# Performance work log

Hardware: AMD Instinct MI355X
Metric: run time of the kernel (lower is better)

Reference implementation:

```python
import jax, jax.numpy as jnp
import numpy as np

T, H, I, E, K, G, TG = 8192, 2048, 1024, 64, 8, 8, 4
ROUTED_SCALE = 2.5


def setup_inputs() -> dict:
    key = jax.random.key(0)
    ks = jax.random.split(key, 7)
    s = 0.02  # weight init scale
    return {
        "hidden_states": jax.random.normal(ks[0], (T, H), jnp.float32),
        "gate_w": jax.random.normal(ks[1], (E, H), jnp.float32) * s,
        "e_bias": jax.random.normal(ks[2], (E,), jnp.float32) * s,
        "w_gate_up": jax.random.normal(ks[3], (E, H, 2 * I), jnp.float32) * s,
        "w_down": jax.random.normal(ks[4], (E, I, H), jnp.float32) * s,
        "shared_gate_up": jax.random.normal(ks[5], (H, 2 * I), jnp.float32) * s,
        "shared_down": jax.random.normal(ks[6], (I, H), jnp.float32) * s,
    }


def silu_and_mul(x):
    g, u = jnp.split(x, 2, axis=-1)
    return jax.nn.silu(g) * u


def grouped_topk(router_logits, e_bias):
    # sigmoid scoring with e_score_correction_bias (DeepSeek-V3 / GLM4-MoE style)
    scores = jax.nn.sigmoid(router_logits)            # [T, E]
    scores_for_choice = scores + e_bias[None, :]
    # group score = sum of top-2 biased scores in each group
    grp = scores_for_choice.reshape(-1, G, E // G)
    group_scores = jax.lax.top_k(grp, 2)[0].sum(-1)   # [T, G]
    _, gidx = jax.lax.top_k(group_scores, TG)         # [T, TG]
    tok = jnp.arange(scores.shape[0])[:, None]
    group_mask = jnp.zeros_like(group_scores, dtype=bool).at[tok, gidx].set(True)
    expert_mask = jnp.repeat(group_mask, E // G, axis=-1)  # [T, E]
    masked = jnp.where(expert_mask, scores_for_choice, -jnp.inf)
    _, topk_ids = jax.lax.top_k(masked, K)            # [T, K]
    # combine weights come from the *unbiased* sigmoid scores
    topk_w = jnp.take_along_axis(scores, topk_ids, axis=-1)
    topk_w = topk_w / jnp.sum(topk_w, axis=-1, keepdims=True)  # renormalize
    return topk_w, topk_ids


def reference(hidden_states, gate_w, e_bias, w_gate_up, w_down,
              shared_gate_up, shared_down):
    x = hidden_states                                  # [T, H]
    # gate runs in fp32
    router_logits = x.astype(jnp.float32) @ gate_w.T   # [T, E]
    topk_w, topk_ids = grouped_topk(router_logits, e_bias)

    # shared expert MLP
    shared_out = silu_and_mul(x @ shared_gate_up) @ shared_down  # [T, H]

    # dense [T, E] combine matrix (top-k sparse in values)
    tok = jnp.arange(x.shape[0])[:, None]
    route = jnp.zeros((x.shape[0], E), x.dtype).at[tok, topk_ids].set(
        topk_w.astype(x.dtype))

    # grouped expert GEMMs via scan over experts (bounds peak memory)
    def body(acc, params):
        w1, w2, rw = params                            # [H,2I], [I,H], [T]
        y = silu_and_mul(x @ w1) @ w2                  # [T, H]
        return acc + rw[:, None] * y, None

    acc0 = jnp.zeros_like(x)
    routed_out, _ = jax.lax.scan(body, acc0, (w_gate_up, w_down, route.T))

    return routed_out * ROUTED_SCALE + shared_out
```

## Files before the change

### kernel.cpp

```cpp
#include <hip/hip_runtime.h>
#include <stdint.h>

#define T_TOK 8192
#define HDIM  2048
#define IDIM  1024
#define NEXP  64
#define KTOP  8
#define TGRP  4
#define TKTOT (T_TOK*KTOP)
#define MAXITEMS 4096
#define RSCALE 2.5f

typedef __attribute__((ext_vector_type(8))) short short8;
typedef __attribute__((ext_vector_type(4))) float f32x4;

#define VMCNT(n) asm volatile("s_waitcnt vmcnt(" #n ")" ::: "memory")
#define BARRIER() asm volatile("s_barrier" ::: "memory")

__device__ __forceinline__ float bf2f(uint16_t u) {
    union { unsigned i; float f; } v; v.i = ((unsigned)u) << 16; return v.f;
}
__device__ __forceinline__ uint16_t f2bf(float f) {
    union { float f; unsigned i; } v; v.f = f;
    unsigned r = (v.i + 0x7FFFu + ((v.i >> 16) & 1u)) >> 16;
    return (uint16_t)r;
}
__device__ __forceinline__ void gload_lds16(const void* g, void* l) {
    __builtin_amdgcn_global_load_lds(
        (const __attribute__((address_space(1))) void*)g,
        (__attribute__((address_space(3))) void*)l, 16, 0, 0);
}
__device__ __forceinline__ int imin(int a, int b) { return a < b ? a : b; }

__global__ __launch_bounds__(256) void k_router(
    const float* __restrict__ x, const float* __restrict__ gw,
    const float* __restrict__ ebias,
    int* __restrict__ topk_ids, float* __restrict__ topk_w,
    int* __restrict__ counts)
{
    __shared__ float xs[16][132];
    __shared__ float wsb[64][133];
    __shared__ float sc[16][65];
    __shared__ float su[16][65];
    const int tid = threadIdx.x;
    const int e = tid & 63;
    const int tg = tid >> 6;
    const long tblk = (long)blockIdx.x * 16;

    float acc0 = 0.f, acc1 = 0.f, acc2 = 0.f, acc3 = 0.f;
    for (int ch = 0; ch < 16; ++ch) {
        const int h0 = ch << 7;
        for (int i = tid; i < 512; i += 256) {
            int r = i >> 5, c4 = (i & 31) << 2;
            float4 v = *(const float4*)(x + (tblk + r) * HDIM + h0 + c4);
            *(float4*)&xs[r][c4] = v;
        }
        for (int i = tid; i < 8192; i += 256) {
            int r = i >> 7, c = i & 127;
            wsb[r][c] = gw[(long)r * HDIM + h0 + c];
        }
        __syncthreads();
        #pragma unroll 8
        for (int hh = 0; hh < 128; ++hh) {
            float wv = wsb[e][hh];
            acc0 += xs[tg][hh] * wv;
            acc1 += xs[tg + 4][hh] * wv;
            acc2 += xs[tg + 8][hh] * wv;
            acc3 += xs[tg + 12][hh] * wv;
        }
        __syncthreads();
    }
    const float be = ebias[e];
    {
        float s;
        s = 1.f / (1.f + expf(-acc0)); su[tg][e] = s;      sc[tg][e] = s + be;
        s = 1.f / (1.f + expf(-acc1)); su[tg + 4][e] = s;  sc[tg + 4][e] = s + be;
        s = 1.f / (1.f + expf(-acc2)); su[tg + 8][e] = s;  sc[tg + 8][e] = s + be;
        s = 1.f / (1.f + expf(-acc3)); su[tg + 12][e] = s; sc[tg + 12][e] = s + be;
    }
    __syncthreads();
    if (tid < 16) {
        const int t = tid;
        float gs[8];
        #pragma unroll
        for (int g = 0; g < 8; ++g) {
            float m1 = -1e30f, m2 = -1e30f;
            #pragma unroll
            for (int j = 0; j < 8; ++j) {
                float v = sc[t][g * 8 + j];
                if (v > m1) { m2 = m1; m1 = v; } else if (v > m2) { m2 = v; }
            }
            gs[g] = m1 + m2;
        }
        int selmask = 0;
        #pragma unroll
        for (int it = 0; it < TGRP; ++it) {
            float best = -1e30f; int bg = 0;
            #pragma unroll
            for (int g = 0; g < 8; ++g)
                if (!((selmask >> g) & 1) && gs[g] > best) { best = gs[g]; bg = g; }
            selmask |= (1 << bg);
        }
        unsigned long long chosen = 0ull;
        int ids[KTOP]; float wv[KTOP]; float wsum = 0.f;
        #pragma unroll
        for (int it = 0; it < KTOP; ++it) {
            float best = -1e30f; int bi = 0;
            for (int ee = 0; ee < 64; ++ee) {
                if (((selmask >> (ee >> 3)) & 1) && !((chosen >> ee) & 1ull)) {
                    float v = sc[t][ee];
                    if (v > best) { best = v; bi = ee; }
                }
            }
            chosen |= (1ull << bi);
            ids[it] = bi; wv[it] = su[t][bi]; wsum += wv[it];
        }
        const float inv = 1.f / wsum;
        #pragma unroll
        for (int k = 0; k < KTOP; ++k) {
            topk_ids[(tblk + t) * KTOP + k] = ids[k];
            topk_w[(tblk + t) * KTOP + k] = wv[k] * inv;
            atomicAdd(&counts[ids[k]], 1);
        }
    }
}

__global__ __launch_bounds__(64) void k_scan2(
    const int* __restrict__ counts, int* offsets, int* cursor,
    int* __restrict__ it_r0, int* __restrict__ it_end,
    int* __restrict__ it_e, int* __restrict__ it_n0, int* __restrict__ nitems)
{
    const int e = threadIdx.x;
    const int c = counts[e];
    int pre = c;
    #pragma unroll
    for (int d = 1; d < 64; d <<= 1) {
        int v = __shfl_up(pre, d, 64);
        if (e >= d) pre += v;
    }
    const int offE = pre - c;
    offsets[e] = offE; cursor[e] = offE;
    const int ntl = (c + 255) >> 8;
    int ipre = ntl;
    #pragma unroll
    for (int d = 1; d < 64; d <<= 1) {
        int v = __shfl_up(ipre, d, 64);
        if (e >= d) ipre += v;
    }
    const int ibase = (ipre - ntl) * 8;
    for (int p = 0; p < 8; ++p)
        for (int t = 0; t < ntl; ++t) {
            int idx = ibase + p * ntl + t;
            it_r0[idx] = offE + t * 256;
            it_end[idx] = offE + c;
            it_e[idx] = e;
            it_n0[idx] = p << 8;
        }
    if (e == 63) *nitems = ibase + ntl * 8;
}

__global__ __launch_bounds__(256) void k_scatter(
    const int* __restrict__ topk_ids, int* cursor,
    int* __restrict__ perm_token, int* __restrict__ slot_of)
{
    int i = blockIdx.x * 256 + threadIdx.x;
    if (i >= TKTOT) return;
    int e = topk_ids[i];
    int pos = atomicAdd(&cursor[e], 1);
    perm_token[pos] = i >> 3;
    slot_of[i] = pos;
}

__global__ __launch_bounds__(256) void k_cvt_bf16(
    const float* __restrict__ in, uint16_t* __restrict__ outp, long n4)
{
    long i = (long)blockIdx.x * 256 + threadIdx.x;
    if (i >= n4) return;
    float4 v = *(const float4*)(in + i * 4);
    uint64_t pk = (uint64_t)f2bf(v.x) | ((uint64_t)f2bf(v.y) << 16)
                | ((uint64_t)f2bf(v.z) << 32) | ((uint64_t)f2bf(v.w) << 48);
    *(uint64_t*)(outp + i * 4) = pk;
}

template<bool INTER>
__global__ __launch_bounds__(256) void k_transpose2(
    const float* __restrict__ src, uint16_t* __restrict__ dst,
    int R, int C, long sStride, long dStride)
{
    __shared__ float tile[64][65];
    const int c0 = blockIdx.x << 6, r0 = blockIdx.y << 6, s = blockIdx.z;
    const float* S = src + (long)s * sStride;
    uint16_t* D = dst + (long)s * dStride;
    const int lc = (threadIdx.x & 15) << 2;
    const int lr = threadIdx.x >> 4;
    #pragma unroll
    for (int p = 0; p < 4; ++p) {
        int y = lr + p * 16;
        float4 v = *(const float4*)(S + (long)(r0 + y) * C + c0 + lc);
        tile[y][lc] = v.x; tile[y][lc + 1] = v.y;
        tile[y][lc + 2] = v.z; tile[y][lc + 3] = v.w;
    }
    __syncthreads();
    const int wc = threadIdx.x >> 3;
    const int wx = (threadIdx.x & 7) << 3;
    #pragma unroll
    for (int p = 0; p < 2; ++p) {
        int c = wc + p * 32;
        short8 v;
        #pragma unroll
        for (int j = 0; j < 8; ++j) v[j] = (short)f2bf(tile[wx + j][c]);
        int cg = c0 + c;
        int rd = INTER ? (((cg & (IDIM - 1)) << 1) + (cg >> 10)) : cg;
        *(short8*)(D + (long)rd * R + r0 + wx) = v;
    }
}

template<bool GATEUP, bool ROUTED>
__global__ __launch_bounds__(512, 2) void k_gemm6(
    const uint16_t* __restrict__ A, const uint16_t* __restrict__ Bw,
    void* __restrict__ OutP,
    const int* __restrict__ perm_token,
    const int* __restrict__ it_r0, const int* __restrict__ it_end,
    const int* __restrict__ it_e, const int* __restrict__ it_n0,
    const int* __restrict__ nitems, int* __restrict__ qcur,
    int Kd, long expStride)
{
    __shared__ char ldsb[4 * 32768];
    __shared__ int s_item;
    const int tid = threadIdx.x, lane = tid & 63, wid = tid >> 6;
    const int wm = wid >> 2, wn = wid & 3;

    const int rchunk = lane >> 2;
    const int swzS = ((lane & 3) ^ ((lane >> 3) & 3)) << 3;
    const int swzR = ((lane >> 4) ^ ((lane >> 1) & 3)) << 4;
    const int aoff = (wm * 128 + (lane & 15)) * 64 + swzR;
    const int boff = (wn * 64 + (lane & 15)) * 64 + swzR;
    const int dstA0 = (wid * 2) * 1024;
    const int dstA1 = (wid * 2 + 1) * 1024;

    const int nKt = Kd >> 5;
    const int NI = ROUTED ? nitems[0] : 0;

    for (;;) {
        int row0, end, n0; long eoff;
        if (ROUTED) {
            __syncthreads();
            if (tid == 0) s_item = atomicAdd(qcur, 1);
            __syncthreads();
            const int it = s_item;
            if (it >= NI) break;
            row0 = it_r0[it]; end = it_end[it]; n0 = it_n0[it];
            eoff = (long)it_e[it] * expStride;
        } else {
            row0 = (int)(blockIdx.x >> 3) << 8;
            end = row0 + 256;
            n0 = (int)(blockIdx.x & 7) << 8;
            eoff = 0;
        }

        const uint16_t *pa0, *pa1, *pb0, *pb1;
        {
            int r0l = wid * 32 + rchunk;
            int r1l = wid * 32 + 16 + rchunk;
            int ra0 = row0 + r0l, ra1 = row0 + r1l;
            if (ROUTED) { ra0 = imin(ra0, end - 1); ra1 = imin(ra1, end - 1); }
            long ga0 = (GATEUP && ROUTED) ? (long)perm_token[ra0] : (long)ra0;
            long ga1 = (GATEUP && ROUTED) ? (long)perm_token[ra1] : (long)ra1;
            pa0 = A + ga0 * Kd + swzS;
            pa1 = A + ga1 * Kd + swzS;
            pb0 = Bw + eoff + (long)(n0 + r0l) * Kd + swzS;
            pb1 = Bw + eoff + (long)(n0 + r1l) * Kd + swzS;
        }

        f32x4 acc[8][4];
        #pragma unroll
        for (int f = 0; f < 8; ++f)
            #pragma unroll
            for (int g = 0; g < 4; ++g) { f32x4 z = {0.f,0.f,0.f,0.f}; acc[f][g] = z; }

        #pragma unroll
        for (int j = 0; j < 3; ++j) {
            char* bb = ldsb + j * 32768;
            gload_lds16(pa0 + (j << 5), bb + dstA0);
            gload_lds16(pa1 + (j << 5), bb + dstA1);
            gload_lds16(pb0 + (j << 5), bb + 16384 + dstA0);
            gload_lds16(pb1 + (j << 5), bb + 16384 + dstA1);
        }

        for (int kt = 0; kt < nKt; ++kt) {
            const char* bb = ldsb + (kt & 3) * 32768;
            char* bs = ldsb + ((kt + 3) & 3) * 32768;
            const bool st = (kt + 3) < nKt;

            VMCNT(8);
            BARRIER();

            short8 fa0 = *(const short8*)(bb + aoff);
            short8 fa1 = *(const short8*)(bb + aoff + 1024);
            short8 fa2 = *(const short8*)(bb + aoff + 2048);
            short8 fa3 = *(const short8*)(bb + aoff + 3072);
            short8 fb0 = *(const short8*)(bb + 16384 + boff);
            short8 fb1 = *(const short8*)(bb + 16384 + boff + 1024);
            short8 fb2 = *(const short8*)(bb + 16384 + boff + 2048);
            short8 fb3 = *(const short8*)(bb + 16384 + boff + 3072);
            if (st) {
                gload_lds16(pa0 + ((kt + 3) << 5), bs + dstA0);
                gload_lds16(pa1 + ((kt + 3) << 5), bs + dstA1);
            }
            BARRIER();
            __builtin_amdgcn_s_setprio(1);
            acc[0][0] = __builtin_amdgcn_mfma_f32_16x16x32_bf16(fa0, fb0, acc[0][0], 0, 0, 0);
            acc[0][1] = __builtin_amdgcn_mfma_f32_16x16x32_bf16(fa0, fb1, acc[0][1], 0, 0, 0);
            acc[0][2] = __builtin_amdgcn_mfma_f32_16x16x32_bf16(fa0, fb2, acc[0][2], 0, 0, 0);
            acc[0][3] = __builtin_amdgcn_mfma_f32_16x16x32_bf16(fa0, fb3, acc[0][3], 0, 0, 0);
            acc[1][0] = __builtin_amdgcn_mfma_f32_16x16x32_bf16(fa1, fb0, acc[1][0], 0, 0, 0);
            acc[1][1] = __builtin_amdgcn_mfma_f32_16x16x32_bf16(fa1, fb1, acc[1][1], 0, 0, 0);
            acc[1][2] = __builtin_amdgcn_mfma_f32_16x16x32_bf16(fa1, fb2, acc[1][2], 0, 0, 0);
            acc[1][3] = __builtin_amdgcn_mfma_f32_16x16x32_bf16(fa1, fb3, acc[1][3], 0, 0, 0);
            acc[2][0] = __builtin_amdgcn_mfma_f32_16x16x32_bf16(fa2, fb0, acc[2][0], 0, 0, 0);
            acc[2][1] = __builtin_amdgcn_mfma_f32_16x16x32_bf16(fa2, fb1, acc[2][1], 0, 0, 0);
            acc[2][2] = __builtin_amdgcn_mfma_f32_16x16x32_bf16(fa2, fb2, acc[2][2], 0, 0, 0);
            acc[2][3] = __builtin_amdgcn_mfma_f32_16x16x32_bf16(fa2, fb3, acc[2][3], 0, 0, 0);
            acc[3][0] = __builtin_amdgcn_mfma_f32_16x16x32_bf16(fa3, fb0, acc[3][0], 0, 0, 0);
            acc[3][1] = __builtin_amdgcn_mfma_f32_16x16x32_bf16(fa3, fb1, acc[3][1], 0, 0, 0);
            acc[3][2] = __builtin_amdgcn_mfma_f32_16x16x32_bf16(fa3, fb2, acc[3][2], 0, 0, 0);
            acc[3][3] = __builtin_amdgcn_mfma_f32_16x16x32_bf16(fa3, fb3, acc[3][3], 0, 0, 0);
            __builtin_amdgcn_s_setprio(0);

            short8 fa4 = *(const short8*)(bb + aoff + 4096);
            short8 fa5 = *(const short8*)(bb + aoff + 5120);
            short8 fa6 = *(const short8*)(bb + aoff + 6144);
            short8 fa7 = *(const short8*)(bb + aoff + 7168);
            if (st) {
                gload_lds16(pb0 + ((kt + 3) << 5), bs + 16384 + dstA0);
                gload_lds16(pb1 + ((kt + 3) << 5), bs + 16384 + dstA1);
            }
            BARRIER();
            __builtin_amdgcn_s_setprio(1);
            acc[4][0] = __builtin_amdgcn_mfma_f32_16x16x32_bf16(fa4, fb0, acc[4][0], 0, 0, 0);
            acc[4][1] = __builtin_amdgcn_mfma_f32_16x16x32_bf16(fa4, fb1, acc[4][1], 0, 0, 0);
            acc[4][2] = __builtin_amdgcn_mfma_f32_16x16x32_bf16(fa4, fb2, acc[4][2], 0, 0, 0);
            acc[4][3] = __builtin_amdgcn_mfma_f32_16x16x32_bf16(fa4, fb3, acc[4][3], 0, 0, 0);
            acc[5][0] = __builtin_amdgcn_mfma_f32_16x16x32_bf16(fa5, fb0, acc[5][0], 0, 0, 0);
            acc[5][1] = __builtin_amdgcn_mfma_f32_16x16x32_bf16(fa5, fb1, acc[5][1], 0, 0, 0);
            acc[5][2] = __builtin_amdgcn_mfma_f32_16x16x32_bf16(fa5, fb2, acc[5][2], 0, 0, 0);
            acc[5][3] = __builtin_amdgcn_mfma_f32_16x16x32_bf16(fa5, fb3, acc[5][3], 0, 0, 0);
            acc[6][0] = __builtin_amdgcn_mfma_f32_16x16x32_bf16(fa6, fb0, acc[6][0], 0, 0, 0);
            acc[6][1] = __builtin_amdgcn_mfma_f32_16x16x32_bf16(fa6, fb1, acc[6][1], 0, 0, 0);
            acc[6][2] = __builtin_amdgcn_mfma_f32_16x16x32_bf16(fa6, fb2, acc[6][2], 0, 0, 0);
            acc[6][3] = __builtin_amdgcn_mfma_f32_16x16x32_bf16(fa6, fb3, acc[6][3], 0, 0, 0);
            acc[7][0] = __builtin_amdgcn_mfma_f32_16x16x32_bf16(fa7, fb0, acc[7][0], 0, 0, 0);
            acc[7][1] = __builtin_amdgcn_mfma_f32_16x16x32_bf16(fa7, fb1, acc[7][1], 0, 0, 0);
            acc[7][2] = __builtin_amdgcn_mfma_f32_16x16x32_bf16(fa7, fb2, acc[7][2], 0, 0, 0);
            acc[7][3] = __builtin_amdgcn_mfma_f32_16x16x32_bf16(fa7, fb3, acc[7][3], 0, 0, 0);
            __builtin_amdgcn_s_setprio(0);
        }

        const int colb = n0 + wn * 64 + (lane & 15);
        const int rowbase = row0 + wm * 128 + ((lane >> 4) << 2);
        if (GATEUP) {
            uint16_t* Oact = (uint16_t*)OutP;
            const bool evenl = ((lane & 1) == 0);
            #pragma unroll
            for (int f = 0; f < 8; ++f)
                #pragma unroll
                for (int g = 0; g < 4; ++g) {
                    f32x4 v = acc[f][g];
                    #pragma unroll
                    for (int r = 0; r < 4; ++r) {
                        float gg = v[r];
                        float uu = __shfl_xor(gg, 1, 64);
                        int row = rowbase + f * 16 + r;
                        if (evenl && (!ROUTED || row < end)) {
                            int jcol = (colb + g * 16) >> 1;
                            float sg = gg / (1.f + __expf(-gg));
                            Oact[(long)row * IDIM + jcol] = f2bf(sg * uu);
                        }
                    }
                }
        } else if (ROUTED) {
            uint16_t* Y = (uint16_t*)OutP;
            #pragma unroll
            for (int f = 0; f < 8; ++f)
                #pragma unroll
                for (int g = 0; g < 4; ++g) {
                    f32x4 v = acc[f][g];
                    #pragma unroll
                    for (int r = 0; r < 4; ++r) {
                        int row = rowbase + f * 16 + r;
                        if (row < end)
                            Y[(long)row * HDIM + colb + g * 16] = f2bf(v[r]);
                    }
                }
        } else {
            float* O = (float*)OutP;
            #pragma unroll
            for (int f = 0; f < 8; ++f)
                #pragma unroll
                for (int g = 0; g < 4; ++g) {
                    f32x4 v = acc[f][g];
                    #pragma unroll
                    for (int r = 0; r < 4; ++r) {
                        int row = rowbase + f * 16 + r;
                        O[(long)row * HDIM + colb + g * 16] = v[r];
                    }
                }
        }
        if (!ROUTED) break;
    }
}

__global__ __launch_bounds__(256) void k_combine(
    float* __restrict__ out, const uint16_t* __restrict__ ybuf,
    const int* __restrict__ slot_of, const float* __restrict__ topk_w)
{
    __shared__ int sl[KTOP];
    __shared__ float sw[KTOP];
    const int t = blockIdx.x, tid = threadIdx.x;
    if (tid < KTOP) {
        sl[tid] = slot_of[t * KTOP + tid];
        sw[tid] = topk_w[t * KTOP + tid] * RSCALE;
    }
    __syncthreads();
    const int h0 = tid << 3;
    float* orow = out + (long)t * HDIM + h0;
    float4 v0 = *(const float4*)(orow);
    float4 v1 = *(const float4*)(orow + 4);
    float a[8] = { v0.x, v0.y, v0.z, v0.w, v1.x, v1.y, v1.z, v1.w };
    #pragma unroll
    for (int k = 0; k < KTOP; ++k) {
        const uint16_t* yr = ybuf + (long)sl[k] * HDIM + h0;
        short8 y = *(const short8*)yr;
        float w = sw[k];
        #pragma unroll
        for (int j = 0; j < 8; ++j)
            a[j] += w * bf2f((uint16_t)y[j]);
    }
    v0.x = a[0]; v0.y = a[1]; v0.z = a[2]; v0.w = a[3];
    v1.x = a[4]; v1.y = a[5]; v1.z = a[6]; v1.w = a[7];
    *(float4*)(orow) = v0;
    *(float4*)(orow + 4) = v1;
}

extern "C" void kernel_launch(void* const* d_in, const int* in_sizes, int n_in,
                              void* d_out, int out_size, void* d_ws, size_t ws_size,
                              hipStream_t stream)
{
    const float* x  = (const float*)d_in[0];
    const float* gw = (const float*)d_in[1];
    const float* eb = (const float*)d_in[2];
    const float* w1 = (const float*)d_in[3];
    const float* w2 = (const float*)d_in[4];
    const float* s1 = (const float*)d_in[5];
    const float* s2 = (const float*)d_in[6];
    float* out = (float*)d_out;
    char* ws = (char*)d_ws;

    size_t off = 0;
    auto take = [&](size_t b) { size_t r = off; off += (b + 255) & ~(size_t)255; return r; };
    const size_t oXBF = take((size_t)T_TOK * HDIM * 2);
    const size_t oACT = take((size_t)TKTOT * IDIM * 2);
    const size_t oASH = take((size_t)T_TOK * IDIM * 2);
    const size_t oW1T = take((size_t)NEXP * 2048 * 2048 * 2);
    const size_t oW2T = take((size_t)NEXP * 2048 * 1024 * 2);
    const size_t oS1T = take((size_t)2048 * 2048 * 2);
    const size_t oS2T = take((size_t)2048 * 1024 * 2);
    const size_t oTKI = take((size_t)TKTOT * 4);
    const size_t oTKW = take((size_t)TKTOT * 4);
    const size_t oSLT = take((size_t)TKTOT * 4);
    const size_t oPRM = take((size_t)TKTOT * 4);
    const size_t oCTL = take(1024);
    const size_t oOFS = take(256);
    const size_t oCUR = take(256);
    const size_t oNT  = take(256);
    const size_t oIR  = take(MAXITEMS * 4);
    const size_t oIE  = take(MAXITEMS * 4);
    const size_t oIX  = take(MAXITEMS * 4);
    const size_t oIN  = take(MAXITEMS * 4);
    (void)ws_size; (void)in_sizes; (void)n_in; (void)out_size;

    uint16_t* xbf  = (uint16_t*)(ws + oXBF);
    uint16_t* act  = (uint16_t*)(ws + oACT);
    uint16_t* ash  = (uint16_t*)(ws + oASH);
    uint16_t* w1t  = (uint16_t*)(ws + oW1T);
    uint16_t* ybuf = (uint16_t*)(ws + oW1T);
    uint16_t* w2t  = (uint16_t*)(ws + oW2T);
    uint16_t* s1t  = (uint16_t*)(ws + oS1T);
    uint16_t* s2t  = (uint16_t*)(ws + oS2T);
    int*   tki  = (int*)(ws + oTKI);
    float* tkw  = (float*)(ws + oTKW);
    int*   slot = (int*)(ws + oSLT);
    int*   prm  = (int*)(ws + oPRM);
    int*   ctl  = (int*)(ws + oCTL);
    int*   ofs  = (int*)(ws + oOFS);
    int*   cur  = (int*)(ws + oCUR);
    int*   nt   = (int*)(ws + oNT);
    int*   ir0  = (int*)(ws + oIR);
    int*   iend = (int*)(ws + oIE);
    int*   ie   = (int*)(ws + oIX);
    int*   in0  = (int*)(ws + oIN);

    hipMemsetAsync(ws + oCTL, 0, 1024, stream);

    k_router<<<T_TOK / 16, 256, 0, stream>>>(x, gw, eb, tki, tkw, ctl);
    k_scan2<<<1, 64, 0, stream>>>(ctl, ofs, cur, ir0, iend, ie, in0, nt);
    k_scatter<<<TKTOT / 256, 256, 0, stream>>>(tki, cur, prm, slot);

    k_cvt_bf16<<<(T_TOK * HDIM / 4 + 255) / 256, 256, 0, stream>>>(x, xbf, (long)T_TOK * HDIM / 4);
    k_transpose2<true ><<<dim3(32, 32, NEXP), 256, 0, stream>>>(w1, w1t, 2048, 2048,
        (long)2048 * 2048, (long)2048 * 2048);
    k_transpose2<false><<<dim3(32, 16, NEXP), 256, 0, stream>>>(w2, w2t, 1024, 2048,
        (long)1024 * 2048, (long)2048 * 1024);
    k_transpose2<true ><<<dim3(32, 32, 1), 256, 0, stream>>>(s1, s1t, 2048, 2048, 0, 0);
    k_transpose2<false><<<dim3(32, 16, 1), 256, 0, stream>>>(s2, s2t, 1024, 2048, 0, 0);

    k_gemm6<true, false><<<dim3(256), 512, 0, stream>>>(
        xbf, s1t, ash, nullptr, nullptr, nullptr, nullptr, nullptr, nullptr, nullptr, 2048, 0);
    k_gemm6<true, true><<<dim3(256), 512, 0, stream>>>(
        xbf, w1t, act, prm, ir0, iend, ie, in0, nt, ctl + 64, 2048, (long)2048 * 2048);
    k_gemm6<false, false><<<dim3(256), 512, 0, stream>>>(
        ash, s2t, out, nullptr, nullptr, nullptr, nullptr, nullptr, nullptr, nullptr, 1024, 0);
    k_gemm6<false, true><<<dim3(256), 512, 0, stream>>>(
        act, w2t, ybuf, nullptr, ir0, iend, ie, in0, nt, ctl + 65, 1024, (long)2048 * 1024);

    k_combine<<<T_TOK, 256, 0, stream>>>(out, ybuf, slot, tkw);
}
```

Baseline: 2.140 ms.

## Shrink GEMM tiles to 128x128 with 256-thread blocks and finer routed work items

Moves the grouped and shared GEMMs from 256x256 tiles on 512-thread blocks to 128x128 tiles on 256-thread blocks. LDS staging and the accumulator arrays are halved, and the routed scheduler splits each expert into 128-row by 128-column items. The aim is less padding waste on experts whose token counts are not multiples of 256, better load balance across CUs, and higher occupancy. The cost is lower arithmetic intensity per tile, with more global and LDS traffic for each MFMA, plus a tail-aware vmcnt wait in the k-loop.

```diff
diff --git a/kernel.cpp b/kernel.cpp
--- a/kernel.cpp
+++ b/kernel.cpp
@@ -8,7 +8,7 @@
 #define KTOP  8
 #define TGRP  4
 #define TKTOT (T_TOK*KTOP)
-#define MAXITEMS 4096
+#define MAXITEMS 12288
 #define RSCALE 2.5f
 
 typedef __attribute__((ext_vector_type(8))) short short8;
@@ -125,7 +125,7 @@
     }
 }
 
-__global__ __launch_bounds__(64) void k_scan2(
+__global__ __launch_bounds__(64) void k_scan3(
     const int* __restrict__ counts, int* offsets, int* cursor,
     int* __restrict__ it_r0, int* __restrict__ it_end,
     int* __restrict__ it_e, int* __restrict__ it_n0, int* __restrict__ nitems)
@@ -140,23 +140,23 @@
     }
     const int offE = pre - c;
     offsets[e] = offE; cursor[e] = offE;
-    const int ntl = (c + 255) >> 8;
+    const int ntl = (c + 127) >> 7;
     int ipre = ntl;
     #pragma unroll
     for (int d = 1; d < 64; d <<= 1) {
         int v = __shfl_up(ipre, d, 64);
         if (e >= d) ipre += v;
     }
-    const int ibase = (ipre - ntl) * 8;
-    for (int p = 0; p < 8; ++p)
+    const int ibase = (ipre - ntl) * 16;
+    for (int p = 0; p < 16; ++p)
         for (int t = 0; t < ntl; ++t) {
             int idx = ibase + p * ntl + t;
-            it_r0[idx] = offE + t * 256;
+            it_r0[idx] = offE + t * 128;
             it_end[idx] = offE + c;
             it_e[idx] = e;
-            it_n0[idx] = p << 8;
-        }
-    if (e == 63) *nitems = ibase + ntl * 8;
+            it_n0[idx] = p << 7;
+        }
+    if (e == 63) *nitems = ibase + ntl * 16;
 }
 
 __global__ __launch_bounds__(256) void k_scatter(
@@ -216,7 +216,7 @@
 }
 
 template<bool GATEUP, bool ROUTED>
-__global__ __launch_bounds__(512, 2) void k_gemm6(
+__global__ __launch_bounds__(256, 2) void k_gemm7(
     const uint16_t* __restrict__ A, const uint16_t* __restrict__ Bw,
     void* __restrict__ OutP,
     const int* __restrict__ perm_token,
@@ -225,18 +225,18 @@
     const int* __restrict__ nitems, int* __restrict__ qcur,
     int Kd, long expStride)
 {
-    __shared__ char ldsb[4 * 32768];
+    __shared__ char ldsb[4 * 16384];
     __shared__ int s_item;
     const int tid = threadIdx.x, lane = tid & 63, wid = tid >> 6;
-    const int wm = wid >> 2, wn = wid & 3;
+    const int wm = wid >> 1, wn = wid & 1;
 
     const int rchunk = lane >> 2;
     const int swzS = ((lane & 3) ^ ((lane >> 3) & 3)) << 3;
     const int swzR = ((lane >> 4) ^ ((lane >> 1) & 3)) << 4;
-    const int aoff = (wm * 128 + (lane & 15)) * 64 + swzR;
+    const int aoff = (wm * 64 + (lane & 15)) * 64 + swzR;
     const int boff = (wn * 64 + (lane & 15)) * 64 + swzR;
-    const int dstA0 = (wid * 2) * 1024;
-    const int dstA1 = (wid * 2 + 1) * 1024;
+    const int dst0 = (wid * 2) * 1024;
+    const int dst1 = (wid * 2 + 1) * 1024;
 
     const int nKt = Kd >> 5;
     const int NI = ROUTED ? nitems[0] : 0;
@@ -252,16 +252,16 @@
             row0 = it_r0[it]; end = it_end[it]; n0 = it_n0[it];
             eoff = (long)it_e[it] * expStride;
         } else {
-            row0 = (int)(blockIdx.x >> 3) << 8;
-            end = row0 + 256;
-            n0 = (int)(blockIdx.x & 7) << 8;
+            row0 = (int)(blockIdx.x >> 4) << 7;
+            end = row0 + 128;
+            n0 = (int)(blockIdx.x & 15) << 7;
             eoff = 0;
         }
 
         const uint16_t *pa0, *pa1, *pb0, *pb1;
         {
             int r0l = wid * 32 + rchunk;
-            int r1l = wid * 32 + 16 + rchunk;
+            int r1l = r0l + 16;
             int ra0 = row0 + r0l, ra1 = row0 + r1l;
             if (ROUTED) { ra0 = imin(ra0, end - 1); ra1 = imin(ra1, end - 1); }
             long ga0 = (GATEUP && ROUTED) ? (long)perm_token[ra0] : (long)ra0;
@@ -272,40 +272,41 @@
             pb1 = Bw + eoff + (long)(n0 + r1l) * Kd + swzS;
         }
 
-        f32x4 acc[8][4];
-        #pragma unroll
-        for (int f = 0; f < 8; ++f)
+        f32x4 acc[4][4];
+        #pragma unroll
+        for (int f = 0; f < 4; ++f)
             #pragma unroll
             for (int g = 0; g < 4; ++g) { f32x4 z = {0.f,0.f,0.f,0.f}; acc[f][g] = z; }
 
         #pragma unroll
         for (int j = 0; j < 3; ++j) {
-            char* bb = ldsb + j * 32768;
-            gload_lds16(pa0 + (j << 5), bb + dstA0);
-            gload_lds16(pa1 + (j << 5), bb + dstA1);
-            gload_lds16(pb0 + (j << 5), bb + 16384 + dstA0);
-            gload_lds16(pb1 + (j << 5), bb + 16384 + dstA1);
+            char* bb = ldsb + j * 16384;
+            gload_lds16(pa0 + (j << 5), bb + dst0);
+            gload_lds16(pa1 + (j << 5), bb + dst1);
+            gload_lds16(pb0 + (j << 5), bb + 8192 + dst0);
+            gload_lds16(pb1 + (j << 5), bb + 8192 + dst1);
         }
 
         for (int kt = 0; kt < nKt; ++kt) {
-            const char* bb = ldsb + (kt & 3) * 32768;
-            char* bs = ldsb + ((kt + 3) & 3) * 32768;
-            const bool st = (kt + 3) < nKt;
-
-            VMCNT(8);
+            if (kt + 2 < nKt)      VMCNT(8);
+            else if (kt + 1 < nKt) VMCNT(4);
+            else                   VMCNT(0);
             BARRIER();
-
+            const char* bb = ldsb + (kt & 3) * 16384;
+            char* bs = ldsb + ((kt + 3) & 3) * 16384;
             short8 fa0 = *(const short8*)(bb + aoff);
             short8 fa1 = *(const short8*)(bb + aoff + 1024);
             short8 fa2 = *(const short8*)(bb + aoff + 2048);
             short8 fa3 = *(const short8*)(bb + aoff + 3072);
-            short8 fb0 = *(const short8*)(bb + 16384 + boff);
-            short8 fb1 = *(const short8*)(bb + 16384 + boff + 1024);
-            short8 fb2 = *(const short8*)(bb + 16384 + boff + 2048);
-            short8 fb3 = *(const short8*)(bb + 16384 + boff + 3072);
-            if (st) {
-                gload_lds16(pa0 + ((kt + 3) << 5), bs + dstA0);
-                gload_lds16(pa1 + ((kt + 3) << 5), bs + dstA1);
+            short8 fb0 = *(const short8*)(bb + 8192 + boff);
+            short8 fb1 = *(const short8*)(bb + 8192 + boff + 1024);
+            short8 fb2 = *(const short8*)(bb + 8192 + boff + 2048);
+            short8 fb3 = *(const short8*)(bb + 8192 + boff + 3072);
+            if (kt + 3 < nKt) {
+                gload_lds16(pa0 + ((kt + 3) << 5), bs + dst0);
+                gload_lds16(pa1 + ((kt + 3) << 5), bs + dst1);
+                gload_lds16(pb0 + ((kt + 3) << 5), bs + 8192 + dst0);
+                gload_lds16(pb1 + ((kt + 3) << 5), bs + 8192 + dst1);
             }
             BARRIER();
             __builtin_amdgcn_s_setprio(1);
@@ -326,43 +327,15 @@
             acc[3][2] = __builtin_amdgcn_mfma_f32_16x16x32_bf16(fa3, fb2, acc[3][2], 0, 0, 0);
             acc[3][3] = __builtin_amdgcn_mfma_f32_16x16x32_bf16(fa3, fb3, acc[3][3], 0, 0, 0);
             __builtin_amdgcn_s_setprio(0);
-
-            short8 fa4 = *(const short8*)(bb + aoff + 4096);
-            short8 fa5 = *(const short8*)(bb + aoff + 5120);
-            short8 fa6 = *(const short8*)(bb + aoff + 6144);
-            short8 fa7 = *(const short8*)(bb + aoff + 7168);
-            if (st) {
-                gload_lds16(pb0 + ((kt + 3) << 5), bs + 16384 + dstA0);
-                gload_lds16(pb1 + ((kt + 3) << 5), bs + 16384 + dstA1);
-            }
-            BARRIER();
-            __builtin_amdgcn_s_setprio(1);
-            acc[4][0] = __builtin_amdgcn_mfma_f32_16x16x32_bf16(fa4, fb0, acc[4][0], 0, 0, 0);
-            acc[4][1] = __builtin_amdgcn_mfma_f32_16x16x32_bf16(fa4, fb1, acc[4][1], 0, 0, 0);
-            acc[4][2] = __builtin_amdgcn_mfma_f32_16x16x32_bf16(fa4, fb2, acc[4][2], 0, 0, 0);
-            acc[4][3] = __builtin_amdgcn_mfma_f32_16x16x32_bf16(fa4, fb3, acc[4][3], 0, 0, 0);
-            acc[5][0] = __builtin_amdgcn_mfma_f32_16x16x32_bf16(fa5, fb0, acc[5][0], 0, 0, 0);
-            acc[5][1] = __builtin_amdgcn_mfma_f32_16x16x32_bf16(fa5, fb1, acc[5][1], 0, 0, 0);
-            acc[5][2] = __builtin_amdgcn_mfma_f32_16x16x32_bf16(fa5, fb2, acc[5][2], 0, 0, 0);
-            acc[5][3] = __builtin_amdgcn_mfma_f32_16x16x32_bf16(fa5, fb3, acc[5][3], 0, 0, 0);
-            acc[6][0] = __builtin_amdgcn_mfma_f32_16x16x32_bf16(fa6, fb0, acc[6][0], 0, 0, 0);
-            acc[6][1] = __builtin_amdgcn_mfma_f32_16x16x32_bf16(fa6, fb1, acc[6][1], 0, 0, 0);
-            acc[6][2] = __builtin_amdgcn_mfma_f32_16x16x32_bf16(fa6, fb2, acc[6][2], 0, 0, 0);
-            acc[6][3] = __builtin_amdgcn_mfma_f32_16x16x32_bf16(fa6, fb3, acc[6][3], 0, 0, 0);
-            acc[7][0] = __builtin_amdgcn_mfma_f32_16x16x32_bf16(fa7, fb0, acc[7][0], 0, 0, 0);
-            acc[7][1] = __builtin_amdgcn_mfma_f32_16x16x32_bf16(fa7, fb1, acc[7][1], 0, 0, 0);
-            acc[7][2] = __builtin_amdgcn_mfma_f32_16x16x32_bf16(fa7, fb2, acc[7][2], 0, 0, 0);
-            acc[7][3] = __builtin_amdgcn_mfma_f32_16x16x32_bf16(fa7, fb3, acc[7][3], 0, 0, 0);
-            __builtin_amdgcn_s_setprio(0);
         }
 
         const int colb = n0 + wn * 64 + (lane & 15);
-        const int rowbase = row0 + wm * 128 + ((lane >> 4) << 2);
+        const int rowbase = row0 + wm * 64 + ((lane >> 4) << 2);
         if (GATEUP) {
             uint16_t* Oact = (uint16_t*)OutP;
             const bool evenl = ((lane & 1) == 0);
             #pragma unroll
-            for (int f = 0; f < 8; ++f)
+            for (int f = 0; f < 4; ++f)
                 #pragma unroll
                 for (int g = 0; g < 4; ++g) {
                     f32x4 v = acc[f][g];
@@ -381,7 +354,7 @@
         } else if (ROUTED) {
             uint16_t* Y = (uint16_t*)OutP;
             #pragma unroll
-            for (int f = 0; f < 8; ++f)
+            for (int f = 0; f < 4; ++f)
                 #pragma unroll
                 for (int g = 0; g < 4; ++g) {
                     f32x4 v = acc[f][g];
@@ -395,7 +368,7 @@
         } else {
             float* O = (float*)OutP;
             #pragma unroll
-            for (int f = 0; f < 8; ++f)
+            for (int f = 0; f < 4; ++f)
                 #pragma unroll
                 for (int g = 0; g < 4; ++g) {
                     f32x4 v = acc[f][g];
@@ -503,7 +476,7 @@
     hipMemsetAsync(ws + oCTL, 0, 1024, stream);
 
     k_router<<<T_TOK / 16, 256, 0, stream>>>(x, gw, eb, tki, tkw, ctl);
-    k_scan2<<<1, 64, 0, stream>>>(ctl, ofs, cur, ir0, iend, ie, in0, nt);
+    k_scan3<<<1, 64, 0, stream>>>(ctl, ofs, cur, ir0, iend, ie, in0, nt);
     k_scatter<<<TKTOT / 256, 256, 0, stream>>>(tki, cur, prm, slot);
 
     k_cvt_bf16<<<(T_TOK * HDIM / 4 + 255) / 256, 256, 0, stream>>>(x, xbf, (long)T_TOK * HDIM / 4);
@@ -514,13 +487,13 @@
     k_transpose2<true ><<<dim3(32, 32, 1), 256, 0, stream>>>(s1, s1t, 2048, 2048, 0, 0);
     k_transpose2<false><<<dim3(32, 16, 1), 256, 0, stream>>>(s2, s2t, 1024, 2048, 0, 0);
 
-    k_gemm6<true, false><<<dim3(256), 512, 0, stream>>>(
+    k_gemm7<true, false><<<dim3(1024), 256, 0, stream>>>(
         xbf, s1t, ash, nullptr, nullptr, nullptr, nullptr, nullptr, nullptr, nullptr, 2048, 0);
-    k_gemm6<true, true><<<dim3(256), 512, 0, stream>>>(
+    k_gemm7<true, true><<<dim3(512), 256, 0, stream>>>(
         xbf, w1t, act, prm, ir0, iend, ie, in0, nt, ctl + 64, 2048, (long)2048 * 2048);
-    k_gemm6<false, false><<<dim3(256), 512, 0, stream>>>(
+    k_gemm7<false, false><<<dim3(1024), 256, 0, stream>>>(
         ash, s2t, out, nullptr, nullptr, nullptr, nullptr, nullptr, nullptr, nullptr, 1024, 0);
-    k_gemm6<false, true><<<dim3(256), 512, 0, stream>>>(
+    k_gemm7<false, true><<<dim3(512), 256, 0, stream>>>(
         act, w2t, ybuf, nullptr, ir0, iend, ie, in0, nt, ctl + 65, 1024, (long)2048 * 1024);
 
     k_combine<<<T_TOK, 256, 0, stream>>>(out, ybuf, slot, tkw);
```

Result: slower. 2.316 ms (+8.2%).

## Use one barrier per k-step and stagger MFMA half-order across waves

Applied to the files above, without the earlier changes.

The GEMM main loop drops from three barriers per k-step to one: all four global-to-LDS prefetches are issued right after the barrier, and the vmcnt wait is tapered in the last iterations so it stays correct when fewer prefetches are in flight. Odd and even waves process the two A-fragment halves in opposite order, which staggers LDS reads against MFMA work across waves. This is meant to cut barrier stalls and LDS read contention. The cost is a larger code body and longer register lifetimes, which could spill at the 2-blocks-per-CU launch bound.

```diff
diff --git a/kernel.cpp b/kernel.cpp
--- a/kernel.cpp
+++ b/kernel.cpp
@@ -216,7 +216,7 @@
 }
 
 template<bool GATEUP, bool ROUTED>
-__global__ __launch_bounds__(512, 2) void k_gemm6(
+__global__ __launch_bounds__(512, 2) void k_gemm8(
     const uint16_t* __restrict__ A, const uint16_t* __restrict__ Bw,
     void* __restrict__ OutP,
     const int* __restrict__ perm_token,
@@ -237,6 +237,7 @@
     const int boff = (wn * 64 + (lane & 15)) * 64 + swzR;
     const int dstA0 = (wid * 2) * 1024;
     const int dstA1 = (wid * 2 + 1) * 1024;
+    const bool oddw = (wid & 1);
 
     const int nKt = Kd >> 5;
     const int NI = ROUTED ? nitems[0] : 0;
@@ -290,70 +291,114 @@
         for (int kt = 0; kt < nKt; ++kt) {
             const char* bb = ldsb + (kt & 3) * 32768;
             char* bs = ldsb + ((kt + 3) & 3) * 32768;
-            const bool st = (kt + 3) < nKt;
-
-            VMCNT(8);
+
+            if (kt + 2 < nKt)      VMCNT(8);
+            else if (kt + 1 < nKt) VMCNT(4);
+            else                   VMCNT(0);
             BARRIER();
-
-            short8 fa0 = *(const short8*)(bb + aoff);
-            short8 fa1 = *(const short8*)(bb + aoff + 1024);
-            short8 fa2 = *(const short8*)(bb + aoff + 2048);
-            short8 fa3 = *(const short8*)(bb + aoff + 3072);
+            if (kt + 3 < nKt) {
+                gload_lds16(pa0 + ((kt + 3) << 5), bs + dstA0);
+                gload_lds16(pa1 + ((kt + 3) << 5), bs + dstA1);
+                gload_lds16(pb0 + ((kt + 3) << 5), bs + 16384 + dstA0);
+                gload_lds16(pb1 + ((kt + 3) << 5), bs + 16384 + dstA1);
+            }
+
             short8 fb0 = *(const short8*)(bb + 16384 + boff);
             short8 fb1 = *(const short8*)(bb + 16384 + boff + 1024);
             short8 fb2 = *(const short8*)(bb + 16384 + boff + 2048);
             short8 fb3 = *(const short8*)(bb + 16384 + boff + 3072);
-            if (st) {
-                gload_lds16(pa0 + ((kt + 3) << 5), bs + dstA0);
-                gload_lds16(pa1 + ((kt + 3) << 5), bs + dstA1);
+
+            if (!oddw) {
+                short8 fa0 = *(const short8*)(bb + aoff);
+                short8 fa1 = *(const short8*)(bb + aoff + 1024);
+                short8 fa2 = *(const short8*)(bb + aoff + 2048);
+                short8 fa3 = *(const short8*)(bb + aoff + 3072);
+                __builtin_amdgcn_s_setprio(1);
+                acc[0][0] = __builtin_amdgcn_mfma_f32_16x16x32_bf16(fa0, fb0, acc[0][0], 0, 0, 0);
+                acc[0][1] = __builtin_amdgcn_mfma_f32_16x16x32_bf16(fa0, fb1, acc[0][1], 0, 0, 0);
+                acc[0][2] = __builtin_amdgcn_mfma_f32_16x16x32_bf16(fa0, fb2, acc[0][2], 0, 0, 0);
+                acc[0][3] = __builtin_amdgcn_mfma_f32_16x16x32_bf16(fa0, fb3, acc[0][3], 0, 0, 0);
+                acc[1][0] = __builtin_amdgcn_mfma_f32_16x16x32_bf16(fa1, fb0, acc[1][0], 0, 0, 0);
+                acc[1][1] = __builtin_amdgcn_mfma_f32_16x16x32_bf16(fa1, fb1, acc[1][1], 0, 0, 0);
+                acc[1][2] = __builtin_amdgcn_mfma_f32_16x16x32_bf16(fa1, fb2, acc[1][2], 0, 0, 0);
+                acc[1][3] = __builtin_amdgcn_mfma_f32_16x16x32_bf16(fa1, fb3, acc[1][3], 0, 0, 0);
+                acc[2][0] = __builtin_amdgcn_mfma_f32_16x16x32_bf16(fa2, fb0, acc[2][0], 0, 0, 0);
+                acc[2][1] = __builtin_amdgcn_mfma_f32_16x16x32_bf16(fa2, fb1, acc[2][1], 0, 0, 0);
+                acc[2][2] = __builtin_amdgcn_mfma_f32_16x16x32_bf16(fa2, fb2, acc[2][2], 0, 0, 0);
+                acc[2][3] = __builtin_amdgcn_mfma_f32_16x16x32_bf16(fa2, fb3, acc[2][3], 0, 0, 0);
+                acc[3][0] = __builtin_amdgcn_mfma_f32_16x16x32_bf16(fa3, fb0, acc[3][0], 0, 0, 0);
+                acc[3][1] = __builtin_amdgcn_mfma_f32_16x16x32_bf16(fa3, fb1, acc[3][1], 0, 0, 0);
+                acc[3][2] = __builtin_amdgcn_mfma_f32_16x16x32_bf16(fa3, fb2, acc[3][2], 0, 0, 0);
+                acc[3][3] = __builtin_amdgcn_mfma_f32_16x16x32_bf16(fa3, fb3, acc[3][3], 0, 0, 0);
+                __builtin_amdgcn_s_setprio(0);
+                short8 fa4 = *(const short8*)(bb + aoff + 4096);
+                short8 fa5 = *(const short8*)(bb + aoff + 5120);
+                short8 fa6 = *(const short8*)(bb + aoff + 6144);
+                short8 fa7 = *(const short8*)(bb + aoff + 7168);
+                __builtin_amdgcn_s_setprio(1);
+                acc[4][0] = __builtin_amdgcn_mfma_f32_16x16x32_bf16(fa4, fb0, acc[4][0], 0, 0, 0);
+                acc[4][1] = __builtin_amdgcn_mfma_f32_16x16x32_bf16(fa4, fb1, acc[4][1], 0, 0, 0);
+                acc[4][2] = __builtin_amdgcn_mfma_f32_16x16x32_bf16(fa4, fb2, acc[4][2], 0, 0, 0);
+                acc[4][3] = __builtin_amdgcn_mfma_f32_16x16x32_bf16(fa4, fb3, acc[4][3], 0, 0, 0);
+                acc[5][0] = __builtin_amdgcn_mfma_f32_16x16x32_bf16(fa5, fb0, acc[5][0], 0, 0, 0);
+                acc[5][1] = __builtin_amdgcn_mfma_f32_16x16x32_bf16(fa5, fb1, acc[5][1], 0, 0, 0);
+                acc[5][2] = __builtin_amdgcn_mfma_f32_16x16x32_bf16(fa5, fb2, acc[5][2], 0, 0, 0);
+                acc[5][3] = __builtin_amdgcn_mfma_f32_16x16x32_bf16(fa5, fb3, acc[5][3], 0, 0, 0);
+                acc[6][0] = __builtin_amdgcn_mfma_f32_16x16x32_bf16(fa6, fb0, acc[6][0], 0, 0, 0);
+                acc[6][1] = __builtin_amdgcn_mfma_f32_16x16x32_bf16(fa6, fb1, acc[6][1], 0, 0, 0);
+                acc[6][2] = __builtin_amdgcn_mfma_f32_16x16x32_bf16(fa6, fb2, acc[6][2], 0, 0, 0);
+                acc[6][3] = __builtin_amdgcn_mfma_f32_16x16x32_bf16(fa6, fb3, acc[6][3], 0, 0, 0);
+                acc[7][0] = __builtin_amdgcn_mfma_f32_16x16x32_bf16(fa7, fb0, acc[7][0], 0, 0, 0);
+                acc[7][1] = __builtin_amdgcn_mfma_f32_16x16x32_bf16(fa7, fb1, acc[7][1], 0, 0, 0);
+                acc[7][2] = __builtin_amdgcn_mfma_f32_16x16x32_bf16(fa7, fb2, acc[7][2], 0, 0, 0);
+                acc[7][3] = __builtin_amdgcn_mfma_f32_16x16x32_bf16(fa7, fb3, acc[7][3], 0, 0, 0);
+                __builtin_amdgcn_s_setprio(0);
+            } else {
+                short8 fa4 = *(const short8*)(bb + aoff + 4096);
+                short8 fa5 = *(const short8*)(bb + aoff + 5120);
+                short8 fa6 = *(const short8*)(bb + aoff + 6144);
+                short8 fa7 = *(const short8*)(bb + aoff + 7168);
+                __builtin_amdgcn_s_setprio(1);
+                acc[4][0] = __builtin_amdgcn_mfma_f32_16x16x32_bf16(fa4, fb0, acc[4][0], 0, 0, 0);
+                acc[4][1] = __builtin_amdgcn_mfma_f32_16x16x32_bf16(fa4, fb1, acc[4][1], 0, 0, 0);
+                acc[4][2] = __builtin_amdgcn_mfma_f32_16x16x32_bf16(fa4, fb2, acc[4][2], 0, 0, 0);
+                acc[4][3] = __builtin_amdgcn_mfma_f32_16x16x32_bf16(fa4, fb3, acc[4][3], 0, 0, 0);
+                acc[5][0] = __builtin_amdgcn_mfma_f32_16x16x32_bf16(fa5, fb0, acc[5][0], 0, 0, 0);
+                acc[5][1] = __builtin_amdgcn_mfma_f32_16x16x32_bf16(fa5, fb1, acc[5][1], 0, 0, 0);
+                acc[5][2] = __builtin_amdgcn_mfma_f32_16x16x32_bf16(fa5, fb2, acc[5][2], 0, 0, 0);
+                acc[5][3] = __builtin_amdgcn_mfma_f32_16x16x32_bf16(fa5, fb3, acc[5][3], 0, 0, 0);
+                acc[6][0] = __builtin_amdgcn_mfma_f32_16x16x32_bf16(fa6, fb0, acc[6][0], 0, 0, 0);
+                acc[6][1] = __builtin_amdgcn_mfma_f32_16x16x32_bf16(fa6, fb1, acc[6][1], 0, 0, 0);
+                acc[6][2] = __builtin_amdgcn_mfma_f32_16x16x32_bf16(fa6, fb2, acc[6][2], 0, 0, 0);
+                acc[6][3] = __builtin_amdgcn_mfma_f32_16x16x32_bf16(fa6, fb3, acc[6][3], 0, 0, 0);
+                acc[7][0] = __builtin_amdgcn_mfma_f32_16x16x32_bf16(fa7, fb0, acc[7][0], 0, 0, 0);
+                acc[7][1] = __builtin_amdgcn_mfma_f32_16x16x32_bf16(fa7, fb1, acc[7][1], 0, 0, 0);
+                acc[7][2] = __builtin_amdgcn_mfma_f32_16x16x32_bf16(fa7, fb2, acc[7][2], 0, 0, 0);
+                acc[7][3] = __builtin_amdgcn_mfma_f32_16x16x32_bf16(fa7, fb3, acc[7][3], 0, 0, 0);
+                __builtin_amdgcn_s_setprio(0);
+                short8 fa0 = *(const short8*)(bb + aoff);
+                short8 fa1 = *(const short8*)(bb + aoff + 1024);
+                short8 fa2 = *(const short8*)(bb + aoff + 2048);
+                short8 fa3 = *(const short8*)(bb + aoff + 3072);
+                __builtin_amdgcn_s_setprio(1);
+                acc[0][0] = __builtin_amdgcn_mfma_f32_16x16x32_bf16(fa0, fb0, acc[0][0], 0, 0, 0);
+                acc[0][1] = __builtin_amdgcn_mfma_f32_16x16x32_bf16(fa0, fb1, acc[0][1], 0, 0, 0);
+                acc[0][2] = __builtin_amdgcn_mfma_f32_16x16x32_bf16(fa0, fb2, acc[0][2], 0, 0, 0);
+                acc[0][3] = __builtin_amdgcn_mfma_f32_16x16x32_bf16(fa0, fb3, acc[0][3], 0, 0, 0);
+                acc[1][0] = __builtin_amdgcn_mfma_f32_16x16x32_bf16(fa1, fb0, acc[1][0], 0, 0, 0);
+                acc[1][1] = __builtin_amdgcn_mfma_f32_16x16x32_bf16(fa1, fb1, acc[1][1], 0, 0, 0);
+                acc[1][2] = __builtin_amdgcn_mfma_f32_16x16x32_bf16(fa1, fb2, acc[1][2], 0, 0, 0);
+                acc[1][3] = __builtin_amdgcn_mfma_f32_16x16x32_bf16(fa1, fb3, acc[1][3], 0, 0, 0);
+                acc[2][0] = __builtin_amdgcn_mfma_f32_16x16x32_bf16(fa2, fb0, acc[2][0], 0, 0, 0);
+                acc[2][1] = __builtin_amdgcn_mfma_f32_16x16x32_bf16(fa2, fb1, acc[2][1], 0, 0, 0);
+                acc[2][2] = __builtin_amdgcn_mfma_f32_16x16x32_bf16(fa2, fb2, acc[2][2], 0, 0, 0);
+                acc[2][3] = __builtin_amdgcn_mfma_f32_16x16x32_bf16(fa2, fb3, acc[2][3], 0, 0, 0);
+                acc[3][0] = __builtin_amdgcn_mfma_f32_16x16x32_bf16(fa3, fb0, acc[3][0], 0, 0, 0);
+                acc[3][1] = __builtin_amdgcn_mfma_f32_16x16x32_bf16(fa3, fb1, acc[3][1], 0, 0, 0);
+                acc[3][2] = __builtin_amdgcn_mfma_f32_16x16x32_bf16(fa3, fb2, acc[3][2], 0, 0, 0);
+                acc[3][3] = __builtin_amdgcn_mfma_f32_16x16x32_bf16(fa3, fb3, acc[3][3], 0, 0, 0);
+                __builtin_amdgcn_s_setprio(0);
             }
-            BARRIER();
-            __builtin_amdgcn_s_setprio(1);
-            acc[0][0] = __builtin_amdgcn_mfma_f32_16x16x32_bf16(fa0, fb0, acc[0][0], 0, 0, 0);
-            acc[0][1] = __builtin_amdgcn_mfma_f32_16x16x32_bf16(fa0, fb1, acc[0][1], 0, 0, 0);
-            acc[0][2] = __builtin_amdgcn_mfma_f32_16x16x32_bf16(fa0, fb2, acc[0][2], 0, 0, 0);
-            acc[0][3] = __builtin_amdgcn_mfma_f32_16x16x32_bf16(fa0, fb3, acc[0][3], 0, 0, 0);
-            acc[1][0] = __builtin_amdgcn_mfma_f32_16x16x32_bf16(fa1, fb0, acc[1][0], 0, 0, 0);
-            acc[1][1] = __builtin_amdgcn_mfma_f32_16x16x32_bf16(fa1, fb1, acc[1][1], 0, 0, 0);
-            acc[1][2] = __builtin_amdgcn_mfma_f32_16x16x32_bf16(fa1, fb2, acc[1][2], 0, 0, 0);
-            acc[1][3] = __builtin_amdgcn_mfma_f32_16x16x32_bf16(fa1, fb3, acc[1][3], 0, 0, 0);
-            acc[2][0] = __builtin_amdgcn_mfma_f32_16x16x32_bf16(fa2, fb0, acc[2][0], 0, 0, 0);
-            acc[2][1] = __builtin_amdgcn_mfma_f32_16x16x32_bf16(fa2, fb1, acc[2][1], 0, 0, 0);
-            acc[2][2] = __builtin_amdgcn_mfma_f32_16x16x32_bf16(fa2, fb2, acc[2][2], 0, 0, 0);
-            acc[2][3] = __builtin_amdgcn_mfma_f32_16x16x32_bf16(fa2, fb3, acc[2][3], 0, 0, 0);
-            acc[3][0] = __builtin_amdgcn_mfma_f32_16x16x32_bf16(fa3, fb0, acc[3][0], 0, 0, 0);
-            acc[3][1] = __builtin_amdgcn_mfma_f32_16x16x32_bf16(fa3, fb1, acc[3][1], 0, 0, 0);
-            acc[3][2] = __builtin_amdgcn_mfma_f32_16x16x32_bf16(fa3, fb2, acc[3][2], 0, 0, 0);
-            acc[3][3] = __builtin_amdgcn_mfma_f32_16x16x32_bf16(fa3, fb3, acc[3][3], 0, 0, 0);
-            __builtin_amdgcn_s_setprio(0);
-
-            short8 fa4 = *(const short8*)(bb + aoff + 4096);
-            short8 fa5 = *(const short8*)(bb + aoff + 5120);
-            short8 fa6 = *(const short8*)(bb + aoff + 6144);
-            short8 fa7 = *(const short8*)(bb + aoff + 7168);
-            if (st) {
-                gload_lds16(pb0 + ((kt + 3) << 5), bs + 16384 + dstA0);
-                gload_lds16(pb1 + ((kt + 3) << 5), bs + 16384 + dstA1);
-            }
-            BARRIER();
-            __builtin_amdgcn_s_setprio(1);
-            acc[4][0] = __builtin_amdgcn_mfma_f32_16x16x32_bf16(fa4, fb0, acc[4][0], 0, 0, 0);
-            acc[4][1] = __builtin_amdgcn_mfma_f32_16x16x32_bf16(fa4, fb1, acc[4][1], 0, 0, 0);
-            acc[4][2] = __builtin_amdgcn_mfma_f32_16x16x32_bf16(fa4, fb2, acc[4][2], 0, 0, 0);
-            acc[4][3] = __builtin_amdgcn_mfma_f32_16x16x32_bf16(fa4, fb3, acc[4][3], 0, 0, 0);
-            acc[5][0] = __builtin_amdgcn_mfma_f32_16x16x32_bf16(fa5, fb0, acc[5][0], 0, 0, 0);
-            acc[5][1] = __builtin_amdgcn_mfma_f32_16x16x32_bf16(fa5, fb1, acc[5][1], 0, 0, 0);
-            acc[5][2] = __builtin_amdgcn_mfma_f32_16x16x32_bf16(fa5, fb2, acc[5][2], 0, 0, 0);
-            acc[5][3] = __builtin_amdgcn_mfma_f32_16x16x32_bf16(fa5, fb3, acc[5][3], 0, 0, 0);
-            acc[6][0] = __builtin_amdgcn_mfma_f32_16x16x32_bf16(fa6, fb0, acc[6][0], 0, 0, 0);
-            acc[6][1] = __builtin_amdgcn_mfma_f32_16x16x32_bf16(fa6, fb1, acc[6][1], 0, 0, 0);
-            acc[6][2] = __builtin_amdgcn_mfma_f32_16x16x32_bf16(fa6, fb2, acc[6][2], 0, 0, 0);
-            acc[6][3] = __builtin_amdgcn_mfma_f32_16x16x32_bf16(fa6, fb3, acc[6][3], 0, 0, 0);
-            acc[7][0] = __builtin_amdgcn_mfma_f32_16x16x32_bf16(fa7, fb0, acc[7][0], 0, 0, 0);
-            acc[7][1] = __builtin_amdgcn_mfma_f32_16x16x32_bf16(fa7, fb1, acc[7][1], 0, 0, 0);
-            acc[7][2] = __builtin_amdgcn_mfma_f32_16x16x32_bf16(fa7, fb2, acc[7][2], 0, 0, 0);
-            acc[7][3] = __builtin_amdgcn_mfma_f32_16x16x32_bf16(fa7, fb3, acc[7][3], 0, 0, 0);
-            __builtin_amdgcn_s_setprio(0);
         }
 
         const int colb = n0 + wn * 64 + (lane & 15);
@@ -514,13 +559,13 @@
     k_transpose2<true ><<<dim3(32, 32, 1), 256, 0, stream>>>(s1, s1t, 2048, 2048, 0, 0);
     k_transpose2<false><<<dim3(32, 16, 1), 256, 0, stream>>>(s2, s2t, 1024, 2048, 0, 0);
 
-    k_gemm6<true, false><<<dim3(256), 512, 0, stream>>>(
+    k_gemm8<true, false><<<dim3(256), 512, 0, stream>>>(
         xbf, s1t, ash, nullptr, nullptr, nullptr, nullptr, nullptr, nullptr, nullptr, 2048, 0);
-    k_gemm6<true, true><<<dim3(256), 512, 0, stream>>>(
+    k_gemm8<true, true><<<dim3(256), 512, 0, stream>>>(
         xbf, w1t, act, prm, ir0, iend, ie, in0, nt, ctl + 64, 2048, (long)2048 * 2048);
-    k_gemm6<false, false><<<dim3(256), 512, 0, stream>>>(
+    k_gemm8<false, false><<<dim3(256), 512, 0, stream>>>(
         ash, s2t, out, nullptr, nullptr, nullptr, nullptr, nullptr, nullptr, nullptr, 1024, 0);
-    k_gemm6<false, true><<<dim3(256), 512, 0, stream>>>(
+    k_gemm8<false, true><<<dim3(256), 512, 0, stream>>>(
         act, w2t, ybuf, nullptr, ir0, iend, ie, in0, nt, ctl + 65, 1024, (long)2048 * 1024);
 
     k_combine<<<T_TOK, 256, 0, stream>>>(out, ybuf, slot, tkw);
```

New measurement: 2.378 ms. 1.11x slower.

## Partition routed work queue per XCD and reorder items for expert locality

Applied to the files above, without the earlier changes.

Work items are reordered so the eight N-tiles of each row tile are adjacent. The single global atomic queue is split into eight per-XCD queues, each covering a contiguous slice of items selected by blockIdx&7. The intent is for blocks on the same XCD to share expert weight and activation tiles through that XCD's L2, and to spread atomic contention across eight counters. The pipeline tail also uses tighter vmcnt waits on the last iterations. The tradeoff is load imbalance, since each XCD's queue is static and a fast XCD cannot take work from a slow one.

```diff
diff --git a/kernel.cpp b/kernel.cpp
--- a/kernel.cpp
+++ b/kernel.cpp
@@ -125,10 +125,11 @@
     }
 }
 
-__global__ __launch_bounds__(64) void k_scan2(
+__global__ __launch_bounds__(64) void k_scan4(
     const int* __restrict__ counts, int* offsets, int* cursor,
     int* __restrict__ it_r0, int* __restrict__ it_end,
-    int* __restrict__ it_e, int* __restrict__ it_n0, int* __restrict__ nitems)
+    int* __restrict__ it_e, int* __restrict__ it_n0,
+    int* __restrict__ nitems, int* __restrict__ qctl)
 {
     const int e = threadIdx.x;
     const int c = counts[e];
@@ -148,15 +149,23 @@
         if (e >= d) ipre += v;
     }
     const int ibase = (ipre - ntl) * 8;
-    for (int p = 0; p < 8; ++p)
-        for (int t = 0; t < ntl; ++t) {
-            int idx = ibase + p * ntl + t;
+    for (int t = 0; t < ntl; ++t)
+        for (int p = 0; p < 8; ++p) {
+            int idx = ibase + t * 8 + p;
             it_r0[idx] = offE + t * 256;
             it_end[idx] = offE + c;
             it_e[idx] = e;
             it_n0[idx] = p << 8;
         }
-    if (e == 63) *nitems = ibase + ntl * 8;
+    const int totTl = __shfl(ipre, 63, 64);
+    const int NI = totTl * 8;
+    if (e == 63) *nitems = NI;
+    if (e < 8) {
+        int s  = (int)(((long)e * NI) / 8);
+        int en = (int)(((long)(e + 1) * NI) / 8);
+        qctl[e] = s;       qctl[8 + e]  = en;
+        qctl[16 + e] = s;  qctl[24 + e] = en;
+    }
 }
 
 __global__ __launch_bounds__(256) void k_scatter(
@@ -216,7 +225,7 @@
 }
 
 template<bool GATEUP, bool ROUTED>
-__global__ __launch_bounds__(512, 2) void k_gemm6(
+__global__ __launch_bounds__(512, 2) void k_gemm9(
     const uint16_t* __restrict__ A, const uint16_t* __restrict__ Bw,
     void* __restrict__ OutP,
     const int* __restrict__ perm_token,
@@ -239,16 +248,18 @@
     const int dstA1 = (wid * 2 + 1) * 1024;
 
     const int nKt = Kd >> 5;
-    const int NI = ROUTED ? nitems[0] : 0;
+    const int xcd = (int)(blockIdx.x & 7);
+    const int myEnd = ROUTED ? qcur[8 + xcd] : 0;
+    int* myCur = qcur + xcd;
 
     for (;;) {
         int row0, end, n0; long eoff;
         if (ROUTED) {
             __syncthreads();
-            if (tid == 0) s_item = atomicAdd(qcur, 1);
+            if (tid == 0) s_item = atomicAdd(myCur, 1);
             __syncthreads();
             const int it = s_item;
-            if (it >= NI) break;
+            if (it >= myEnd) break;
             row0 = it_r0[it]; end = it_end[it]; n0 = it_n0[it];
             eoff = (long)it_e[it] * expStride;
         } else {
@@ -292,7 +303,9 @@
             char* bs = ldsb + ((kt + 3) & 3) * 32768;
             const bool st = (kt + 3) < nKt;
 
-            VMCNT(8);
+            if (kt + 2 < nKt)      VMCNT(8);
+            else if (kt + 1 < nKt) VMCNT(4);
+            else                   VMCNT(0);
             BARRIER();
 
             short8 fa0 = *(const short8*)(bb + aoff);
@@ -499,11 +512,12 @@
     int*   iend = (int*)(ws + oIE);
     int*   ie   = (int*)(ws + oIX);
     int*   in0  = (int*)(ws + oIN);
+    int*   qctl = ctl + 64;
 
     hipMemsetAsync(ws + oCTL, 0, 1024, stream);
 
     k_router<<<T_TOK / 16, 256, 0, stream>>>(x, gw, eb, tki, tkw, ctl);
-    k_scan2<<<1, 64, 0, stream>>>(ctl, ofs, cur, ir0, iend, ie, in0, nt);
+    k_scan4<<<1, 64, 0, stream>>>(ctl, ofs, cur, ir0, iend, ie, in0, nt, qctl);
     k_scatter<<<TKTOT / 256, 256, 0, stream>>>(tki, cur, prm, slot);
 
     k_cvt_bf16<<<(T_TOK * HDIM / 4 + 255) / 256, 256, 0, stream>>>(x, xbf, (long)T_TOK * HDIM / 4);
@@ -514,14 +528,14 @@
     k_transpose2<true ><<<dim3(32, 32, 1), 256, 0, stream>>>(s1, s1t, 2048, 2048, 0, 0);
     k_transpose2<false><<<dim3(32, 16, 1), 256, 0, stream>>>(s2, s2t, 1024, 2048, 0, 0);
 
-    k_gemm6<true, false><<<dim3(256), 512, 0, stream>>>(
-        xbf, s1t, ash, nullptr, nullptr, nullptr, nullptr, nullptr, nullptr, nullptr, 2048, 0);
-    k_gemm6<true, true><<<dim3(256), 512, 0, stream>>>(
-        xbf, w1t, act, prm, ir0, iend, ie, in0, nt, ctl + 64, 2048, (long)2048 * 2048);
-    k_gemm6<false, false><<<dim3(256), 512, 0, stream>>>(
-        ash, s2t, out, nullptr, nullptr, nullptr, nullptr, nullptr, nullptr, nullptr, 1024, 0);
-    k_gemm6<false, true><<<dim3(256), 512, 0, stream>>>(
-        act, w2t, ybuf, nullptr, ir0, iend, ie, in0, nt, ctl + 65, 1024, (long)2048 * 1024);
+    k_gemm9<true, false><<<dim3(256), 512, 0, stream>>>(
+        xbf, s1t, ash, nullptr, nullptr, nullptr, nullptr, nullptr, nullptr, qctl, 2048, 0);
+    k_gemm9<true, true><<<dim3(256), 512, 0, stream>>>(
+        xbf, w1t, act, prm, ir0, iend, ie, in0, nt, qctl, 2048, (long)2048 * 2048);
+    k_gemm9<false, false><<<dim3(256), 512, 0, stream>>>(
+        ash, s2t, out, nullptr, nullptr, nullptr, nullptr, nullptr, nullptr, qctl, 1024, 0);
+    k_gemm9<false, true><<<dim3(256), 512, 0, stream>>>(
+        act, w2t, ybuf, nullptr, ir0, iend, ie, in0, nt, qctl + 16, 1024, (long)2048 * 1024);
 
     k_combine<<<T_TOK, 256, 0, stream>>>(out, ybuf, slot, tkw);
 }
```

Result: no change. 2.130 ms (-0.5%).
